# Optimization experiments

Measured on AMD Instinct MI355X. Metric: run time of the kernel, lower is better.

Reference implementation:

```python
import jax, jax.numpy as jnp
import numpy as np

B, S, H = 2, 2048, 1024
NH, HD = 16, 64
WINDOW = 512
NEG = -10000.0


def setup_inputs() -> dict:
    key = jax.random.key(0)
    ks = jax.random.split(key, 8)
    sc = 0.02
    return {
        "hidden_states": jax.random.normal(ks[0], (B, S, H), dtype=jnp.float32),
        "attention_mask": jnp.zeros((B, 1, 1, S), dtype=jnp.float32),
        "Wq": jax.random.normal(ks[1], (H, H), dtype=jnp.float32) * sc,
        "bq": jnp.zeros((H,), dtype=jnp.float32),
        "Wk": jax.random.normal(ks[2], (H, H), dtype=jnp.float32) * sc,
        "bk": jnp.zeros((H,), dtype=jnp.float32),
        "Wv": jax.random.normal(ks[3], (H, H), dtype=jnp.float32) * sc,
        "bv": jnp.zeros((H,), dtype=jnp.float32),
    }


def _heads(x):
    # [b, t, (h d)] -> [b, h, t, d]
    b, t, _ = x.shape
    return x.reshape(b, t, NH, HD).transpose(0, 2, 1, 3)


def reference(hidden_states, attention_mask, Wq, bq, Wk, bk, Wv, bv):
    q = _heads(hidden_states @ Wq.T + bq)
    k = _heads(hidden_states @ Wk.T + bk)
    v = _heads(hidden_states @ Wv.T + bv)

    # Faithful mask construction (note: window mask is triu(diag=-WINDOW),
    # penalizing the recent window, exactly as in the source).
    i = jnp.arange(S)[:, None]
    j = jnp.arange(S)[None, :]
    causal_mask = jnp.where(j > i, NEG, 0.0).astype(jnp.float32)          # triu, diag=1
    window_mask = jnp.where(j >= i - WINDOW, NEG, 0.0).astype(jnp.float32)  # triu, diag=-512
    mask = causal_mask + window_mask + attention_mask  # [b,1,S,S]

    scale = 1.0 / jnp.sqrt(jnp.asarray(HD, dtype=q.dtype))
    scores = jnp.einsum("bhtd,bhsd->bhts", q, k) * scale + mask  # [b,h,S,S]
    probs = jax.nn.softmax(scores, axis=-1)
    out = jnp.einsum("bhts,bhsd->bhtd", probs, v)  # [b,h,S,d]
    # [b,h,t,d] -> [b,t,(h d)]
    return out.transpose(0, 2, 1, 3).reshape(B, S, H)
```

## Files before the change

### kernel.cpp

```cpp
#include <hip/hip_runtime.h>

typedef float f32x2 __attribute__((ext_vector_type(2)));
typedef float f32x4 __attribute__((ext_vector_type(4)));
typedef float f32x16 __attribute__((ext_vector_type(16)));
typedef _Float16 half8 __attribute__((ext_vector_type(8)));
typedef _Float16 half4 __attribute__((ext_vector_type(4)));
typedef unsigned int u32;
typedef u32 u32x4 __attribute__((ext_vector_type(4)));

#define S_LEN 2048
#define NHEAD 16
#define HDIM 64
#define BATCH 2
#define WINDOW 512
#define M2_FIX 5.770780163555852f
#define LOG2E 1.4426950408889634f

#define GLDS16(gp, lp) __builtin_amdgcn_global_load_lds( \
    (const __attribute__((address_space(1))) void*)(gp), \
    (__attribute__((address_space(3))) void*)(lp), 16, 0, 0)


__global__ __launch_bounds__(256) void convert_kernel(
    const float4* __restrict__ hs, const float4* __restrict__ wq,
    const float4* __restrict__ wk, const float4* __restrict__ wv,
    _Float16* __restrict__ hsb, _Float16* __restrict__ wb) {
  int i = blockIdx.x * 256 + threadIdx.x;
  float4 v;
  _Float16* dst;
  if (i < 1048576) {
    v = hs[i];
    dst = hsb + (size_t)i * 4;
  } else {
    int j = i - 1048576;
    if (j < 262144) v = wq[j];
    else if (j < 524288) v = wk[j - 262144];
    else v = wv[j - 524288];
    dst = wb + (size_t)j * 4;
  }
  half4 o;
  o[0] = (_Float16)v.x; o[1] = (_Float16)v.y;
  o[2] = (_Float16)v.z; o[3] = (_Float16)v.w;
  *(half4*)dst = o;
}

__global__ __launch_bounds__(512) void qkv_gemm(
    const _Float16* __restrict__ A, const _Float16* __restrict__ W,
    const float* __restrict__ bq, const float* __restrict__ bk,
    const float* __restrict__ bv,
    _Float16* __restrict__ Qf, _Float16* __restrict__ Kf, _Float16* __restrict__ Vf) {
  __shared__ _Float16 sbuf[2][24576];
  const int tid = threadIdx.x;
  const int wv = tid >> 6;
  const int lane = tid & 63;
  const int g = lane >> 4;
  const int c = lane & 15;
  const int b = blockIdx.x;
  const int xcd = b & 7;
  const int s = b >> 3;
  const int m0 = ((xcd >> 2) * 8 + (s & 7)) * 256;
  const int n0 = ((xcd & 3) * 6 + (s >> 3)) * 128;
  const int wm = (wv & 3) * 64;
  const int wn = (wv >> 2) * 64;

  const int srow8 = lane >> 3;
  const int sslot = lane & 7;
  const int lsl = sslot ^ srow8;
  const _Float16* aS = A + (size_t)(m0 + wv * 32 + srow8) * 1024 + lsl * 8;
  const _Float16* bS = W + (size_t)(n0 + wv * 16 + srow8) * 1024 + lsl * 8;
  const int aBase = wv * 2048;
  const int bBase = 16384 + wv * 1024;

  f32x4 acc[4][4];
#pragma unroll
  for (int i = 0; i < 4; ++i)
#pragma unroll
    for (int j = 0; j < 4; ++j) acc[i][j] = (f32x4){0.f, 0.f, 0.f, 0.f};

  auto STAGE = [&](int bf_, int k0) __attribute__((always_inline)) {
    char* aD = (char*)&sbuf[bf_][aBase];
    char* bD = (char*)&sbuf[bf_][bBase];
#pragma unroll
    for (int grp = 0; grp < 4; ++grp)
      GLDS16(aS + grp * 8192 + k0, aD + grp * 1024);
#pragma unroll
    for (int grp = 0; grp < 2; ++grp)
      GLDS16(bS + grp * 8192 + k0, bD + grp * 1024);
  };

  auto COMPUTE = [&](int bf_) __attribute__((always_inline)) {
    const _Float16* Asb = &sbuf[bf_][0];
    const _Float16* Bsb = &sbuf[bf_][16384];
    half8 af[4][2];
#pragma unroll
    for (int mf = 0; mf < 4; ++mf) {
      const int row = wm + mf * 16 + c;
#pragma unroll
      for (int ch = 0; ch < 2; ++ch)
        af[mf][ch] = *(const half8*)&Asb[row * 64 + ((ch * 4 + g) ^ (c & 7)) * 8];
    }
    __builtin_amdgcn_s_setprio(1);
#pragma unroll
    for (int nf = 0; nf < 4; ++nf) {
      const int row = wn + nf * 16 + c;
      half8 bf0 = *(const half8*)&Bsb[row * 64 + ((g) ^ (c & 7)) * 8];
      half8 bf1 = *(const half8*)&Bsb[row * 64 + ((4 + g) ^ (c & 7)) * 8];
#pragma unroll
      for (int mf = 0; mf < 4; ++mf) {
        acc[mf][nf] = __builtin_amdgcn_mfma_f32_16x16x32_f16(af[mf][0], bf0, acc[mf][nf], 0, 0, 0);
        acc[mf][nf] = __builtin_amdgcn_mfma_f32_16x16x32_f16(af[mf][1], bf1, acc[mf][nf], 0, 0, 0);
      }
    }
    __builtin_amdgcn_s_setprio(0);
  };

  STAGE(0, 0);
  int cur = 0;
  for (int t = 0; t < 15; ++t) {
    STAGE(cur ^ 1, (t + 1) * 64);
    asm volatile("s_waitcnt vmcnt(6)" ::: "memory");
    __builtin_amdgcn_sched_barrier(0);
    __builtin_amdgcn_s_barrier();
    __builtin_amdgcn_sched_barrier(0);
    COMPUTE(cur);
    __builtin_amdgcn_sched_barrier(0);
    __builtin_amdgcn_s_barrier();
    cur ^= 1;
  }
  asm volatile("s_waitcnt vmcnt(0)" ::: "memory");
  __builtin_amdgcn_sched_barrier(0);
  __builtin_amdgcn_s_barrier();
  __builtin_amdgcn_sched_barrier(0);
  COMPUTE(cur);
  __builtin_amdgcn_sched_barrier(0);
  __builtin_amdgcn_s_barrier();

  const int kind = n0 >> 10;
  const int nb = (n0 + wn) & 1023;
  const int head = nb >> 6;
  const float* bias = kind == 0 ? bq : (kind == 1 ? bk : bv);
  _Float16* dst = kind == 0 ? Qf : (kind == 1 ? Kf : Vf);
  _Float16* ob = &sbuf[0][0] + wv * 4096;

  if (kind < 2) {
    const float scl = kind == 0 ? (0.125f * LOG2E) : 1.0f;
#pragma unroll
    for (int nf = 0; nf < 4; ++nf) {
      const int d = nf * 16 + c;
      const float bsv = bias[nb + d];
      const int base = nf * 512 + ((c >> 3) & 1) * 256 + (c & 7);
#pragma unroll
      for (int mf = 0; mf < 4; ++mf) {
#pragma unroll
        for (int r = 0; r < 4; ++r) {
          ob[(mf >> 1) * 2048 + base + (mf & 1) * 128 + g * 32 + r * 8] =
              (_Float16)((acc[mf][nf][r] + bsv) * scl);
        }
      }
    }
  } else {
#pragma unroll
    for (int nf = 0; nf < 4; ++nf) {
      const int d = nf * 16 + c;
      const float bsv = bias[nb + d];
#pragma unroll
      for (int mf = 0; mf < 4; ++mf) {
        half4 v4;
#pragma unroll
        for (int r = 0; r < 4; ++r) v4[r] = (_Float16)(acc[mf][nf][r] + bsv);
        *(half4*)&ob[(mf >> 1) * 2048 + ((nf >> 1) * 2 + (mf & 1)) * 512 +
                     ((g >> 1) * 32 + (nf & 1) * 16 + c) * 8 + (g & 1) * 4] = v4;
      }
    }
  }

  const int bI = (m0 + wm) >> 11;
  const size_t gbase = (size_t)(bI * NHEAD + head) * 131072 +
                       (size_t)(((m0 + wm) & 2047) >> 5) * 2048;
#pragma unroll
  for (int i = 0; i < 8; ++i) {
    half8 v = *(const half8*)&ob[i * 512 + lane * 8];
    *(half8*)&dst[gbase + i * 512 + lane * 8] = v;
  }
}

__global__ __launch_bounds__(256) void attn_kernel(
    const _Float16* __restrict__ Qf, const _Float16* __restrict__ Kf,
    const _Float16* __restrict__ Vf, const float* __restrict__ amask,
    float* __restrict__ out) {
  __shared__ _Float16 obuf[4][32][72];
  __shared__ float lbuf[4][32];
  const int tid = threadIdx.x;
  const int w = tid >> 6;
  const int lane = tid & 63;
  const int q31 = lane & 31;
  const int h = lane >> 5;
  const int bid = blockIdx.x;
  const int bh = bid & 31;
  const int idx = 63 - (bid >> 5);
  const int i0 = idx * 32;
  const int bI = bh >> 4;
  const int head = bh & 15;

  const _Float16* Qh = Qf + (size_t)bh * 131072;
  const _Float16* Kh = Kf + (size_t)bh * 131072;
  const _Float16* Vh = Vf + (size_t)bh * 131072;
  const float* am = amask + (size_t)bI * S_LEN;

  const int q = i0 + q31;
  const int hiq = (q <= WINDOW) ? q : (q - WINDOW - 1);
  const int last = i0 + 31;
  const int himax = (last <= WINDOW) ? last
                    : ((i0 <= WINDOW) ? WINDOW : (last - WINDOW - 1));
  const int hiq_min = (last <= WINDOW) ? i0
                      : ((i0 > WINDOW) ? (i0 - WINDOW - 1) : 0);
  const int ntiles = (himax >> 5) + 1;
  const int nfull = (hiq_min + 1) >> 5;
  const int lim = hiq - 4 * h;

  half8 qf[4];
#pragma unroll
  for (int ch = 0; ch < 4; ++ch)
    qf[ch] = *(const half8*)&Qh[(size_t)idx * 2048 + ch * 512 + lane * 8];

  f32x16 zero16, m2init;
#pragma unroll
  for (int r = 0; r < 16; ++r) { zero16[r] = 0.f; m2init[r] = -M2_FIX; }
  f32x16 oacc0 = zero16, oacc1 = zero16;
  f32x2 lp[4];
#pragma unroll
  for (int r = 0; r < 4; ++r) lp[r] = (f32x2){0.f, 0.f};

  auto computeTile = [&](half8 k0, half8 k1, half8 k2, half8 k3,
                         half8 vf0, half8 vf1, half8 vf2, half8 vf3,
                         f32x4 am0, f32x4 am1, f32x4 am2, f32x4 am3, int t)
      __attribute__((always_inline)) {
    const int j0 = t * 32;
    f32x4 amv[4] = {am0, am1, am2, am3};

    __builtin_amdgcn_s_setprio(1);
    f32x16 st = __builtin_amdgcn_mfma_f32_32x32x16_f16(k0, qf[0], m2init, 0, 0, 0);
    st = __builtin_amdgcn_mfma_f32_32x32x16_f16(k1, qf[1], st, 0, 0, 0);
    st = __builtin_amdgcn_mfma_f32_32x32x16_f16(k2, qf[2], st, 0, 0, 0);
    st = __builtin_amdgcn_mfma_f32_32x32x16_f16(k3, qf[3], st, 0, 0, 0);
    __builtin_amdgcn_s_setprio(0);

    float p[16];
#pragma unroll
    for (int r = 0; r < 16; ++r)
      p[r] = __builtin_fmaf(amv[r >> 2][r & 3], LOG2E, st[r]);
    if (t >= nfull) {
      const int lm = lim - j0;
#pragma unroll
      for (int r = 0; r < 16; ++r) {
        const int off = (r & 3) + 8 * (r >> 2);
        p[r] = (off <= lm) ? p[r] : -3e38f;
      }
    }
#pragma unroll
    for (int r = 0; r < 16; ++r) p[r] = __builtin_amdgcn_exp2f(p[r]);
#pragma unroll
    for (int j = 0; j < 4; ++j) {
      lp[j] += (f32x2){p[2 * j], p[2 * j + 1]};
      lp[j] += (f32x2){p[8 + 2 * j], p[9 + 2 * j]};
    }

    u32 pk[8];
#pragma unroll
    for (int r = 0; r < 8; ++r) {
      auto c2 = __builtin_amdgcn_cvt_pkrtz(p[2 * r], p[2 * r + 1]);
      pk[r] = __builtin_bit_cast(u32, c2);
    }
    u32 a0 = pk[0], b0 = pk[2];
    u32 a1 = pk[1], b1 = pk[3];
    u32 a2 = pk[4], b2 = pk[6];
    u32 a3 = pk[5], b3 = pk[7];
    asm("v_permlane32_swap_b32 %0, %1" : "+v"(a0), "+v"(b0));
    asm("v_permlane32_swap_b32 %0, %1" : "+v"(a1), "+v"(b1));
    asm("v_permlane32_swap_b32 %0, %1" : "+v"(a2), "+v"(b2));
    asm("v_permlane32_swap_b32 %0, %1" : "+v"(a3), "+v"(b3));
    const half8 pf0 = __builtin_bit_cast(half8, (u32x4){a0, a1, b0, b1});
    const half8 pf1 = __builtin_bit_cast(half8, (u32x4){a2, a3, b2, b3});

    __builtin_amdgcn_s_setprio(1);
    oacc0 = __builtin_amdgcn_mfma_f32_32x32x16_f16(vf0, pf0, oacc0, 0, 0, 0);
    oacc0 = __builtin_amdgcn_mfma_f32_32x32x16_f16(vf1, pf1, oacc0, 0, 0, 0);
    oacc1 = __builtin_amdgcn_mfma_f32_32x32x16_f16(vf2, pf0, oacc1, 0, 0, 0);
    oacc1 = __builtin_amdgcn_mfma_f32_32x32x16_f16(vf3, pf1, oacc1, 0, 0, 0);
    __builtin_amdgcn_s_setprio(0);
  };

#define LOADALL(k0, k1, k2, k3, v0, v1, v2, v3, a0_, a1_, a2_, a3_, tt)  \
  {                                                                      \
    const _Float16* kt = Kh + (size_t)(tt) * 2048 + lane * 8;            \
    const _Float16* vt = Vh + (size_t)(tt) * 2048 + lane * 8;            \
    const float* at = am + (tt) * 32 + 4 * h;                            \
    k0 = *(const half8*)&kt[0];                                          \
    k1 = *(const half8*)&kt[512];                                        \
    k2 = *(const half8*)&kt[1024];                                       \
    k3 = *(const half8*)&kt[1536];                                       \
    v0 = *(const half8*)&vt[0];                                          \
    v1 = *(const half8*)&vt[512];                                        \
    v2 = *(const half8*)&vt[1024];                                       \
    v3 = *(const half8*)&vt[1536];                                       \
    a0_ = *(const f32x4*)&at[0];                                         \
    a1_ = *(const f32x4*)&at[8];                                         \
    a2_ = *(const f32x4*)&at[16];                                        \
    a3_ = *(const f32x4*)&at[24];                                        \
  }

  int t = w;
  if (t < ntiles) {
    half8 k0, k1, k2, k3, v0, v1, v2, v3;
    f32x4 a0, a1, a2, a3;
    LOADALL(k0, k1, k2, k3, v0, v1, v2, v3, a0, a1, a2, a3, t);
    int tn = t + 4;
    while (tn < ntiles) {
      half8 n0, n1, n2, n3, u0, u1, u2, u3;
      f32x4 e0, e1, e2, e3;
      LOADALL(n0, n1, n2, n3, u0, u1, u2, u3, e0, e1, e2, e3, tn);
      computeTile(k0, k1, k2, k3, v0, v1, v2, v3, a0, a1, a2, a3, t);
      k0 = n0; k1 = n1; k2 = n2; k3 = n3;
      v0 = u0; v1 = u1; v2 = u2; v3 = u3;
      a0 = e0; a1 = e1; a2 = e2; a3 = e3;
      t = tn;
      tn += 4;
    }
    computeTile(k0, k1, k2, k3, v0, v1, v2, v3, a0, a1, a2, a3, t);
  }

  f32x2 s2 = (lp[0] + lp[1]) + (lp[2] + lp[3]);
  float lw = s2[0] + s2[1];
  lw += __shfl_xor(lw, 32);
  if (h == 0) lbuf[w][q31] = lw;
#pragma unroll
  for (int j = 0; j < 4; ++j) {
    half4 h0, h1;
#pragma unroll
    for (int e = 0; e < 4; ++e) {
      h0[e] = (_Float16)oacc0[4 * j + e];
      h1[e] = (_Float16)oacc1[4 * j + e];
    }
    *(half4*)&obuf[w][q31][4 * h + 8 * j]      = h0;
    *(half4*)&obuf[w][q31][32 + 4 * h + 8 * j] = h1;
  }
  __syncthreads();

  const int mq = tid >> 3;
  const int md = (tid & 7) * 8;
  const float lt = (lbuf[0][mq] + lbuf[1][mq]) + (lbuf[2][mq] + lbuf[3][mq]);
  float s[8];
  half8 p0 = *(const half8*)&obuf[0][mq][md];
#pragma unroll
  for (int e = 0; e < 8; ++e) s[e] = (float)p0[e];
#pragma unroll
  for (int w4 = 1; w4 < 4; ++w4) {
    half8 pw = *(const half8*)&obuf[w4][mq][md];
#pragma unroll
    for (int e = 0; e < 8; ++e) s[e] += (float)pw[e];
  }
  const float inv = 1.0f / lt;
  float4 s0, s1;
  s0.x = s[0] * inv; s0.y = s[1] * inv; s0.z = s[2] * inv; s0.w = s[3] * inv;
  s1.x = s[4] * inv; s1.y = s[5] * inv; s1.z = s[6] * inv; s1.w = s[7] * inv;
  float* op = out + ((size_t)(bI * S_LEN + i0 + mq)) * 1024 + head * 64 + md;
  *(float4*)op = s0;
  *(float4*)(op + 4) = s1;
}

extern "C" void kernel_launch(void* const* d_in, const int* in_sizes, int n_in,
                              void* d_out, int out_size, void* d_ws, size_t ws_size,
                              hipStream_t stream) {
  const float* hs = (const float*)d_in[0];
  const float* am = (const float*)d_in[1];
  const float* Wq = (const float*)d_in[2];
  const float* bq = (const float*)d_in[3];
  const float* Wk = (const float*)d_in[4];
  const float* bk = (const float*)d_in[5];
  const float* Wv = (const float*)d_in[6];
  const float* bv = (const float*)d_in[7];
  float* out = (float*)d_out;

  char* ws = (char*)d_ws;
  _Float16* hsb = (_Float16*)(ws);
  _Float16* wb  = (_Float16*)(ws + 8388608);
  _Float16* Qf  = (_Float16*)(ws + 14680064);
  _Float16* Kf  = (_Float16*)(ws + 23068672);
  _Float16* Vf  = (_Float16*)(ws + 31457280);

  convert_kernel<<<7168, 256, 0, stream>>>(
      (const float4*)hs, (const float4*)Wq, (const float4*)Wk, (const float4*)Wv, hsb, wb);
  qkv_gemm<<<384, 512, 0, stream>>>(hsb, wb, bq, bk, bv, Qf, Kf, Vf);
  attn_kernel<<<2048, 256, 0, stream>>>(Qf, Kf, Vf, am, out);
}
```

Before: 79.31 us.

## Enlarge QKV GEMM tile to 256x256 with interleaved staging and MFMA

The QKV projection GEMM switches from 256x128 tiles on 384 blocks to 256x256 tiles on 192 blocks. Each wave now owns a 128x64 sub-tile with 32 accumulators. The next K-slice's global-to-LDS loads are split into four phases, each interleaved with a quarter of the MFMA work, with a barrier per phase. The goal is more data reuse per LDS load and better overlap of loads with compute, at the cost of fewer blocks than the 256 CUs, more registers, 128KB of LDS per block, and more barriers.

```diff
diff --git a/kernel.cpp b/kernel.cpp
--- a/kernel.cpp
+++ b/kernel.cpp
@@ -44,103 +44,115 @@
   *(half4*)dst = o;
 }
 
-__global__ __launch_bounds__(512) void qkv_gemm(
+__global__ __launch_bounds__(512, 2) void qkv_gemm(
     const _Float16* __restrict__ A, const _Float16* __restrict__ W,
     const float* __restrict__ bq, const float* __restrict__ bk,
     const float* __restrict__ bv,
     _Float16* __restrict__ Qf, _Float16* __restrict__ Kf, _Float16* __restrict__ Vf) {
-  __shared__ _Float16 sbuf[2][24576];
+  __shared__ _Float16 sbuf[65536];
   const int tid = threadIdx.x;
   const int wv = tid >> 6;
   const int lane = tid & 63;
   const int g = lane >> 4;
   const int c = lane & 15;
-  const int b = blockIdx.x;
-  const int xcd = b & 7;
-  const int s = b >> 3;
-  const int m0 = ((xcd >> 2) * 8 + (s & 7)) * 256;
-  const int n0 = ((xcd & 3) * 6 + (s >> 3)) * 128;
-  const int wm = (wv & 3) * 64;
-  const int wn = (wv >> 2) * 64;
-
-  const int srow8 = lane >> 3;
-  const int sslot = lane & 7;
-  const int lsl = sslot ^ srow8;
-  const _Float16* aS = A + (size_t)(m0 + wv * 32 + srow8) * 1024 + lsl * 8;
-  const _Float16* bS = W + (size_t)(n0 + wv * 16 + srow8) * 1024 + lsl * 8;
-  const int aBase = wv * 2048;
-  const int bBase = 16384 + wv * 1024;
-
-  f32x4 acc[4][4];
-#pragma unroll
-  for (int i = 0; i < 4; ++i)
+  const int bid = blockIdx.x;
+  const int m0 = (bid & 15) * 256;
+  const int n0 = (bid >> 4) * 256;
+  const int wm = wv >> 2;
+  const int wn = wv & 3;
+
+  const int srow = tid >> 3;
+  const int sk = ((tid & 7) ^ ((tid >> 3) & 7)) * 8;
+  const _Float16* aSrc = A + (size_t)(m0 + srow) * 1024 + sk;
+  const _Float16* bSrc = W + (size_t)(n0 + srow) * 1024 + sk;
+  char* const ldsB = (char*)&sbuf[0];
+
+  auto STAGE_A = [&](int bf_, int k0, int grp) __attribute__((always_inline)) {
+    GLDS16(aSrc + (size_t)grp * 65536 + k0,
+           ldsB + bf_ * 32768 + grp * 8192 + tid * 16);
+  };
+  auto STAGE_B = [&](int bf_, int k0, int grp) __attribute__((always_inline)) {
+    GLDS16(bSrc + (size_t)grp * 65536 + k0,
+           ldsB + 65536 + bf_ * 32768 + grp * 8192 + tid * 16);
+  };
+
+  const int slot0 = ((0 * 4 + g) ^ (c & 7)) * 8;
+  const int slot1 = ((1 * 4 + g) ^ (c & 7)) * 8;
+  const int aRow = wm * 128 + c;
+  const int bRow = wn * 64 + c;
+
+  f32x4 acc[8][4];
+#pragma unroll
+  for (int i = 0; i < 8; ++i)
 #pragma unroll
     for (int j = 0; j < 4; ++j) acc[i][j] = (f32x4){0.f, 0.f, 0.f, 0.f};
 
-  auto STAGE = [&](int bf_, int k0) __attribute__((always_inline)) {
-    char* aD = (char*)&sbuf[bf_][aBase];
-    char* bD = (char*)&sbuf[bf_][bBase];
-#pragma unroll
-    for (int grp = 0; grp < 4; ++grp)
-      GLDS16(aS + grp * 8192 + k0, aD + grp * 1024);
-#pragma unroll
-    for (int grp = 0; grp < 2; ++grp)
-      GLDS16(bS + grp * 8192 + k0, bD + grp * 1024);
-  };
-
-  auto COMPUTE = [&](int bf_) __attribute__((always_inline)) {
-    const _Float16* Asb = &sbuf[bf_][0];
-    const _Float16* Bsb = &sbuf[bf_][16384];
-    half8 af[4][2];
-#pragma unroll
-    for (int mf = 0; mf < 4; ++mf) {
-      const int row = wm + mf * 16 + c;
-#pragma unroll
-      for (int ch = 0; ch < 2; ++ch)
-        af[mf][ch] = *(const half8*)&Asb[row * 64 + ((ch * 4 + g) ^ (c & 7)) * 8];
-    }
-    __builtin_amdgcn_s_setprio(1);
-#pragma unroll
-    for (int nf = 0; nf < 4; ++nf) {
-      const int row = wn + nf * 16 + c;
-      half8 bf0 = *(const half8*)&Bsb[row * 64 + ((g) ^ (c & 7)) * 8];
-      half8 bf1 = *(const half8*)&Bsb[row * 64 + ((4 + g) ^ (c & 7)) * 8];
-#pragma unroll
-      for (int mf = 0; mf < 4; ++mf) {
-        acc[mf][nf] = __builtin_amdgcn_mfma_f32_16x16x32_f16(af[mf][0], bf0, acc[mf][nf], 0, 0, 0);
-        acc[mf][nf] = __builtin_amdgcn_mfma_f32_16x16x32_f16(af[mf][1], bf1, acc[mf][nf], 0, 0, 0);
-      }
-    }
-    __builtin_amdgcn_s_setprio(0);
-  };
-
-  STAGE(0, 0);
-  int cur = 0;
-  for (int t = 0; t < 15; ++t) {
-    STAGE(cur ^ 1, (t + 1) * 64);
-    asm volatile("s_waitcnt vmcnt(6)" ::: "memory");
-    __builtin_amdgcn_sched_barrier(0);
-    __builtin_amdgcn_s_barrier();
-    __builtin_amdgcn_sched_barrier(0);
-    COMPUTE(cur);
-    __builtin_amdgcn_sched_barrier(0);
-    __builtin_amdgcn_s_barrier();
-    cur ^= 1;
-  }
+#pragma unroll
+  for (int grp = 0; grp < 4; ++grp) STAGE_A(0, 0, grp);
+#pragma unroll
+  for (int grp = 0; grp < 4; ++grp) STAGE_B(0, 0, grp);
   asm volatile("s_waitcnt vmcnt(0)" ::: "memory");
   __builtin_amdgcn_sched_barrier(0);
   __builtin_amdgcn_s_barrier();
-  __builtin_amdgcn_sched_barrier(0);
-  COMPUTE(cur);
-  __builtin_amdgcn_sched_barrier(0);
-  __builtin_amdgcn_s_barrier();
-
-  const int kind = n0 >> 10;
-  const int nb = (n0 + wn) & 1023;
+
+  half8 bfr[4][2];
+  for (int t = 0; t < 16; ++t) {
+    const int bf = t & 1;
+    const int abase = bf * 16384;
+    const int bbase = 32768 + bf * 16384;
+    const int kn = (t + 1) * 64;
+    const bool st = t < 15;
+
+#pragma unroll
+    for (int p = 0; p < 4; ++p) {
+      if (st) {
+        if (p == 0)      { STAGE_A(bf ^ 1, kn, 0); STAGE_A(bf ^ 1, kn, 1); }
+        else if (p == 1) { STAGE_A(bf ^ 1, kn, 2); STAGE_A(bf ^ 1, kn, 3); }
+        else if (p == 2) { STAGE_B(bf ^ 1, kn, 0); STAGE_B(bf ^ 1, kn, 1); }
+        else             { STAGE_B(bf ^ 1, kn, 2); STAGE_B(bf ^ 1, kn, 3); }
+      }
+      if (p == 0) {
+#pragma unroll
+        for (int nf = 0; nf < 4; ++nf) {
+          bfr[nf][0] = *(const half8*)&sbuf[bbase + (bRow + nf * 16) * 64 + slot0];
+          bfr[nf][1] = *(const half8*)&sbuf[bbase + (bRow + nf * 16) * 64 + slot1];
+        }
+      }
+      half8 aq[2][2];
+#pragma unroll
+      for (int mi = 0; mi < 2; ++mi) {
+        const int row = aRow + (2 * p + mi) * 16;
+        aq[mi][0] = *(const half8*)&sbuf[abase + row * 64 + slot0];
+        aq[mi][1] = *(const half8*)&sbuf[abase + row * 64 + slot1];
+      }
+      asm volatile("s_waitcnt lgkmcnt(0)" ::: "memory");
+      __builtin_amdgcn_sched_barrier(0);
+      __builtin_amdgcn_s_setprio(1);
+#pragma unroll
+      for (int nf = 0; nf < 4; ++nf)
+#pragma unroll
+        for (int mi = 0; mi < 2; ++mi) {
+          acc[2 * p + mi][nf] = __builtin_amdgcn_mfma_f32_16x16x32_f16(
+              aq[mi][0], bfr[nf][0], acc[2 * p + mi][nf], 0, 0, 0);
+          acc[2 * p + mi][nf] = __builtin_amdgcn_mfma_f32_16x16x32_f16(
+              aq[mi][1], bfr[nf][1], acc[2 * p + mi][nf], 0, 0, 0);
+        }
+      __builtin_amdgcn_s_setprio(0);
+      if (p == 3) {
+        asm volatile("s_waitcnt vmcnt(0)" ::: "memory");
+        __builtin_amdgcn_sched_barrier(0);
+      }
+      __builtin_amdgcn_s_barrier();
+    }
+  }
+
+  const int nAbs = n0 + wn * 64;
+  const int kind = nAbs >> 10;
+  const int nb = nAbs & 1023;
   const int head = nb >> 6;
   const float* bias = kind == 0 ? bq : (kind == 1 ? bk : bv);
   _Float16* dst = kind == 0 ? Qf : (kind == 1 ? Kf : Vf);
-  _Float16* ob = &sbuf[0][0] + wv * 4096;
+  _Float16* ob = &sbuf[wv * 8192];
 
   if (kind < 2) {
     const float scl = kind == 0 ? (0.125f * LOG2E) : 1.0f;
@@ -150,7 +162,7 @@
       const float bsv = bias[nb + d];
       const int base = nf * 512 + ((c >> 3) & 1) * 256 + (c & 7);
 #pragma unroll
-      for (int mf = 0; mf < 4; ++mf) {
+      for (int mf = 0; mf < 8; ++mf) {
 #pragma unroll
         for (int r = 0; r < 4; ++r) {
           ob[(mf >> 1) * 2048 + base + (mf & 1) * 128 + g * 32 + r * 8] =
@@ -164,7 +176,7 @@
       const int d = nf * 16 + c;
       const float bsv = bias[nb + d];
 #pragma unroll
-      for (int mf = 0; mf < 4; ++mf) {
+      for (int mf = 0; mf < 8; ++mf) {
         half4 v4;
 #pragma unroll
         for (int r = 0; r < 4; ++r) v4[r] = (_Float16)(acc[mf][nf][r] + bsv);
@@ -174,11 +186,12 @@
     }
   }
 
-  const int bI = (m0 + wm) >> 11;
+  const int mRow = m0 + wm * 128;
+  const int bI = mRow >> 11;
   const size_t gbase = (size_t)(bI * NHEAD + head) * 131072 +
-                       (size_t)(((m0 + wm) & 2047) >> 5) * 2048;
-#pragma unroll
-  for (int i = 0; i < 8; ++i) {
+                       (size_t)((mRow & 2047) >> 5) * 2048;
+#pragma unroll
+  for (int i = 0; i < 16; ++i) {
     half8 v = *(const half8*)&ob[i * 512 + lane * 8];
     *(half8*)&dst[gbase + i * 512 + lane * 8] = v;
   }
@@ -390,6 +403,6 @@
 
   convert_kernel<<<7168, 256, 0, stream>>>(
       (const float4*)hs, (const float4*)Wq, (const float4*)Wk, (const float4*)Wv, hsb, wb);
-  qkv_gemm<<<384, 512, 0, stream>>>(hsb, wb, bq, bk, bv, Qf, Kf, Vf);
+  qkv_gemm<<<192, 512, 0, stream>>>(hsb, wb, bq, bk, bv, Qf, Kf, Vf);
   attn_kernel<<<2048, 256, 0, stream>>>(Qf, Kf, Vf, am, out);
 }
```

After: 74.37 us. -6.2%, faster.
